# Kernel optimization log

Hardware: AMD Instinct MI355X
Metric: run time of the kernel (lower is better)

## Reference

```python
import jax, jax.numpy as jnp
import numpy as np

B, T, D_IN, H, C = 256, 2048, 64, 32, 16
RHO, SPARSITY = 0.9, 0.1


def _reservoir(rng, n):
    # uniform(-1,1), scale to spectral radius RHO, then sparsify (same order as torch code)
    W = rng.uniform(-1.0, 1.0, (n, n)).astype(np.float32)
    W *= RHO / np.max(np.abs(np.linalg.eigvals(W)))
    W *= (rng.random((n, n)) < SPARSITY).astype(np.float32)
    return jnp.asarray(W)


def _linear(rng, fan_in, fan_out):
    bound = 1.0 / np.sqrt(fan_in)
    W = rng.uniform(-bound, bound, (fan_out, fan_in)).astype(np.float32)
    b = rng.uniform(-bound, bound, (fan_out,)).astype(np.float32)
    return jnp.asarray(W), jnp.asarray(b)


def setup_inputs() -> dict:
    key = jax.random.key(0)
    rng = np.random.default_rng(0)
    x = jax.random.normal(key, (B, T, D_IN), dtype=jnp.float32)
    # frozen encoder input / reservoir weights (uniform(-1,1) weights, default-init biases)
    W_in = jnp.asarray(rng.uniform(-1.0, 1.0, (H, D_IN)).astype(np.float32))
    b_in = jnp.asarray(rng.uniform(-1 / np.sqrt(D_IN), 1 / np.sqrt(D_IN), (H,)).astype(np.float32))
    W_res_enc = _reservoir(rng, H)
    b_res_enc = jnp.asarray(rng.uniform(-1 / np.sqrt(H), 1 / np.sqrt(H), (H,)).astype(np.float32))
    W_code, b_code = _linear(rng, H, C)
    W_co, b_co = _linear(rng, C, H)
    W_res_dec = _reservoir(rng, H)
    b_res_dec = jnp.asarray(rng.uniform(-1 / np.sqrt(H), 1 / np.sqrt(H), (H,)).astype(np.float32))
    W_ro, b_ro = _linear(rng, H, D_IN)
    return dict(x=x, W_in=W_in, b_in=b_in, W_res_enc=W_res_enc, b_res_enc=b_res_enc,
                W_code=W_code, b_code=b_code, W_co=W_co, b_co=b_co,
                W_res_dec=W_res_dec, b_res_dec=b_res_dec, W_ro=W_ro, b_ro=b_ro)


def reference(x, W_in, b_in, W_res_enc, b_res_enc, W_code, b_code, W_co, b_co,
              W_res_dec, b_res_dec, W_ro, b_ro):
    Bs = x.shape[0]
    h0 = jnp.zeros((Bs, W_res_enc.shape[0]), dtype=x.dtype)
    # precompute input projection for all timesteps: [T, B, H]
    u_enc = jnp.swapaxes(jnp.einsum('btd,hd->bth', x, W_in) + b_in, 0, 1)

    def enc_step(h, u):
        h = jnp.tanh(u + h @ W_res_enc.T + b_res_enc)
        return h, h

    _, enc = jax.lax.scan(enc_step, h0, u_enc)
    enc = jnp.swapaxes(enc, 0, 1)                      # [B, T, H]

    z = enc @ W_code.T + b_code                        # [B, T, C]
    h_dec_in = z @ W_co.T + b_co                       # [B, T, H]

    def dec_step(h, u):
        h = jnp.tanh(u + h @ W_res_dec.T + b_res_dec)
        return h, h

    _, dec = jax.lax.scan(dec_step, h0, jnp.swapaxes(h_dec_in, 0, 1))
    dec = jnp.swapaxes(dec, 0, 1)                      # [B, T, H]
    return dec @ W_ro.T + b_ro                         # [B, T, D_IN]
```

## Files before the change

### kernel.cpp

```cpp
#include <hip/hip_runtime.h>
#include <math.h>

#define B_    256
#define T_    2048
#define DIN   64
#define H_    32
#define C_    16

#define CHUNK 128
#define WARM  96
#define NCHUNK (T_ / CHUNK)

#define OFF_WCOMB 0u
#define OFF_BCOMB 4096u
#define OFF_U     (1u << 20)

__device__ __forceinline__ float fast_tanh(float x) {
    float e2 = __expf(x + x);
    return 1.0f - 2.0f * __builtin_amdgcn_rcpf(e2 + 1.0f);
}

__global__ __launch_bounds__(1024) void prep_kernel(
        const float* __restrict__ W_code, const float* __restrict__ b_code,
        const float* __restrict__ W_co,   const float* __restrict__ b_co,
        float* __restrict__ W_comb, float* __restrict__ b_comb) {
    int t = threadIdx.x;
    int i = t >> 5, j = t & 31;
    float s = 0.0f;
#pragma unroll
    for (int c = 0; c < C_; ++c)
        s += W_co[i * C_ + c] * W_code[c * H_ + j];
    W_comb[i * H_ + j] = s;
    if (t < H_) {
        float sb = b_co[t];
#pragma unroll
        for (int c = 0; c < C_; ++c)
            sb += W_co[t * C_ + c] * b_code[c];
        b_comb[t] = sb;
    }
}

__global__ __launch_bounds__(256) void inproj_kernel(
        const float* __restrict__ x, const float* __restrict__ W_in,
        const float* __restrict__ b_in, const float* __restrict__ b_res_enc,
        float* __restrict__ u) {
    __shared__ __align__(16) float4 lx[128 * 16];

    int tid  = threadIdx.x;
    int w    = tid >> 6;
    int lane = tid & 63;
    int i    = lane & 31;
    int par  = lane >> 5;

    float Wr[DIN];
    {
        const float4* wi4 = reinterpret_cast<const float4*>(W_in + i * DIN);
#pragma unroll
        for (int q = 0; q < DIN / 4; ++q) {
            float4 v = wi4[q];
            Wr[4*q+0] = v.x; Wr[4*q+1] = v.y; Wr[4*q+2] = v.z; Wr[4*q+3] = v.w;
        }
    }
    float bi = b_in[i] + b_res_enc[i];

    long row_base = (long)blockIdx.x * 128;
    const float4* xg = reinterpret_cast<const float4*>(x) + row_base * 16;

#pragma unroll
    for (int k = 0; k < 8; ++k)
        lx[tid + 256 * k] = xg[tid + 256 * k];
    __syncthreads();

#pragma unroll
    for (int g = 0; g < 4; ++g) {
        int r0 = w * 32 + g * 8 + par;
        float acc0 = 0.f, acc1 = 0.f, acc2 = 0.f, acc3 = 0.f;
#pragma unroll
        for (int k4 = 0; k4 < 16; ++k4) {
            float4 wv = { Wr[4*k4+0], Wr[4*k4+1], Wr[4*k4+2], Wr[4*k4+3] };
            float4 x0 = lx[(r0 + 0) * 16 + k4];
            float4 x1 = lx[(r0 + 2) * 16 + k4];
            float4 x2 = lx[(r0 + 4) * 16 + k4];
            float4 x3 = lx[(r0 + 6) * 16 + k4];
            acc0 += x0.x * wv.x + x0.y * wv.y + x0.z * wv.z + x0.w * wv.w;
            acc1 += x1.x * wv.x + x1.y * wv.y + x1.z * wv.z + x1.w * wv.w;
            acc2 += x2.x * wv.x + x2.y * wv.y + x2.z * wv.z + x2.w * wv.w;
            acc3 += x3.x * wv.x + x3.y * wv.y + x3.z * wv.z + x3.w * wv.w;
        }
        long rg = row_base + r0;
        u[(rg + 0) * H_ + i] = acc0 + bi;
        u[(rg + 2) * H_ + i] = acc1 + bi;
        u[(rg + 4) * H_ + i] = acc2 + bi;
        u[(rg + 6) * H_ + i] = acc3 + bi;
    }
}

__device__ __forceinline__ float mv32(const float (&W)[H_], const float (&h)[H_],
                                      float init) {
    float a0 = init, a1 = 0.f, a2 = 0.f, a3 = 0.f;
#pragma unroll
    for (int j = 0; j < H_; j += 4) {
        a0 += W[j+0] * h[j+0];
        a1 += W[j+1] * h[j+1];
        a2 += W[j+2] * h[j+2];
        a3 += W[j+3] * h[j+3];
    }
    return (a0 + a1) + (a2 + a3);
}

__device__ __forceinline__ void gather32(const float (&src)[H_], float (&h)[H_]) {
#pragma unroll
    for (int q = 0; q < H_ / 4; ++q) {
        float4 v = *reinterpret_cast<const float4*>(&src[4 * q]);
        h[4*q+0] = v.x; h[4*q+1] = v.y; h[4*q+2] = v.z; h[4*q+3] = v.w;
    }
}

__device__ __forceinline__ void readout2(const float (&Wo0)[H_], const float (&Wo1)[H_],
                                         float bo0, float bo1, const float (&hd)[H_],
                                         float* dst) {
    float s00 = bo0, s01 = 0.f, s10 = bo1, s11 = 0.f;
#pragma unroll
    for (int j = 0; j < H_; j += 2) {
        s00 += Wo0[j]     * hd[j];
        s01 += Wo0[j + 1] * hd[j + 1];
        s10 += Wo1[j]     * hd[j];
        s11 += Wo1[j + 1] * hd[j + 1];
    }
    *reinterpret_cast<float2*>(dst) = make_float2(s00 + s01, s10 + s11);
}

__global__ __launch_bounds__(64, 2) void scan_kernel(
        const float* __restrict__ u,
        const float* __restrict__ W_res_enc,
        const float* __restrict__ W_res_dec, const float* __restrict__ b_res_dec,
        const float* __restrict__ W_comb,    const float* __restrict__ b_comb,
        const float* __restrict__ W_ro,      const float* __restrict__ b_ro,
        float* __restrict__ out) {
    int lane = threadIdx.x;
    int i = lane & 31;
    int half = lane >> 5;
    int b  = ((blockIdx.x & 127) << 1) | half;
    int c  = blockIdx.x >> 7;
    int t0 = c * CHUNK;
    int tstart = (c == 0) ? 0 : (t0 - WARM);
    int tend = t0 + CHUNK;

    float We[H_], Wc[H_], Wd[H_], Wo0[H_], Wo1[H_];
    {
        const float4* we4 = reinterpret_cast<const float4*>(W_res_enc + i * H_);
        const float4* wc4 = reinterpret_cast<const float4*>(W_comb + i * H_);
        const float4* wd4 = reinterpret_cast<const float4*>(W_res_dec + i * H_);
        const float4* wo0 = reinterpret_cast<const float4*>(W_ro + (2 * i) * H_);
        const float4* wo1 = reinterpret_cast<const float4*>(W_ro + (2 * i + 1) * H_);
#pragma unroll
        for (int q = 0; q < H_ / 4; ++q) {
            float4 a = we4[q], bq = wc4[q], d = wd4[q], o0 = wo0[q], o1 = wo1[q];
            We[4*q+0]=a.x;  We[4*q+1]=a.y;  We[4*q+2]=a.z;  We[4*q+3]=a.w;
            Wc[4*q+0]=bq.x; Wc[4*q+1]=bq.y; Wc[4*q+2]=bq.z; Wc[4*q+3]=bq.w;
            Wd[4*q+0]=d.x;  Wd[4*q+1]=d.y;  Wd[4*q+2]=d.z;  Wd[4*q+3]=d.w;
            Wo0[4*q+0]=o0.x;Wo0[4*q+1]=o0.y;Wo0[4*q+2]=o0.z;Wo0[4*q+3]=o0.w;
            Wo1[4*q+0]=o1.x;Wo1[4*q+1]=o1.y;Wo1[4*q+2]=o1.z;Wo1[4*q+3]=o1.w;
        }
    }
    float bcd = b_comb[i] + b_res_dec[i];
    float bo0 = b_ro[2 * i], bo1 = b_ro[2 * i + 1];

    float henc[H_], hdec[H_];
#pragma unroll
    for (int j = 0; j < H_; ++j) { henc[j] = 0.0f; hdec[j] = 0.0f; }

    __shared__ __align__(16) float lhe[2][H_];
    __shared__ __align__(16) float lhd[2][H_];

    const float* ub = u + ((long)b * T_) * H_ + i;
    float*       ob = out + ((long)b * T_) * DIN + 2 * i;

    float ucur = ub[(long)tstart * H_];
    float un1  = ub[(long)(tstart + 1) * H_];

    for (int t = tstart; t < t0; ++t) {
        float a = fast_tanh(mv32(We, henc, ucur));
        lhe[half][i] = a;
        gather32(lhe[half], henc);
        float dacc = mv32(Wd, hdec, 0.f);
        ucur = un1;
        un1 = ub[(t + 2) * H_];
        float d = fast_tanh(mv32(Wc, henc, bcd) + dacc);
        lhd[half][i] = d;
        gather32(lhd[half], hdec);
    }

    {
        float a = fast_tanh(mv32(We, henc, ucur));
        lhe[half][i] = a;
        gather32(lhe[half], henc);
        float dacc = mv32(Wd, hdec, 0.f);
        ucur = un1;
        un1 = ub[(t0 + 2) * H_];
        float d = fast_tanh(mv32(Wc, henc, bcd) + dacc);
        lhd[half][i] = d;
        gather32(lhd[half], hdec);
    }

    for (int t = t0 + 1; t < tend; ++t) {
        float a = fast_tanh(mv32(We, henc, ucur));
        lhe[half][i] = a;
        gather32(lhe[half], henc);
        float dacc = mv32(Wd, hdec, 0.f);
        readout2(Wo0, Wo1, bo0, bo1, hdec, ob + (long)(t - 1) * DIN);
        int tn = (t + 2 < tend) ? (t + 2) : (tend - 1);
        ucur = un1;
        un1 = ub[tn * H_];
        float d = fast_tanh(mv32(Wc, henc, bcd) + dacc);
        lhd[half][i] = d;
        gather32(lhd[half], hdec);
    }
    readout2(Wo0, Wo1, bo0, bo1, hdec, ob + (long)(tend - 1) * DIN);
}

extern "C" void kernel_launch(void* const* d_in, const int* in_sizes, int n_in,
                              void* d_out, int out_size, void* d_ws, size_t ws_size,
                              hipStream_t stream) {
    const float* x         = (const float*)d_in[0];
    const float* W_in      = (const float*)d_in[1];
    const float* b_in      = (const float*)d_in[2];
    const float* W_res_enc = (const float*)d_in[3];
    const float* b_res_enc = (const float*)d_in[4];
    const float* W_code    = (const float*)d_in[5];
    const float* b_code    = (const float*)d_in[6];
    const float* W_co      = (const float*)d_in[7];
    const float* b_co      = (const float*)d_in[8];
    const float* W_res_dec = (const float*)d_in[9];
    const float* b_res_dec = (const float*)d_in[10];
    const float* W_ro      = (const float*)d_in[11];
    const float* b_ro      = (const float*)d_in[12];
    float* out = (float*)d_out;

    char* ws = (char*)d_ws;
    float* W_comb = (float*)(ws + OFF_WCOMB);
    float* b_comb = (float*)(ws + OFF_BCOMB);
    float* u      = (float*)(ws + OFF_U);

    prep_kernel<<<1, 1024, 0, stream>>>(W_code, b_code, W_co, b_co, W_comb, b_comb);
    inproj_kernel<<<(B_ * T_) / 128, 256, 0, stream>>>(x, W_in, b_in, b_res_enc, u);
    scan_kernel<<<(B_ / 2) * NCHUNK, 64, 0, stream>>>(u, W_res_enc,
                                                      W_res_dec, b_res_dec,
                                                      W_comb, b_comb, W_ro, b_ro, out);
}
```

Baseline: 541.7 us.

## Split readout projection out of the scan into a separate output-projection kernel

Removes the per-step 64-wide readout from the latency-bound recurrent scan. The scan now writes the decoder hidden state into the first 32 floats of each output row, and a new kernel reads those back, applies W_ro and overwrites the row in place. This shortens the serial critical path and frees registers (launch bounds relaxed to 1 block per SIMD hint), and the input prefetch is deepened to three steps. The cost is an extra kernel launch plus a write and re-read of the hidden states through global memory. The in-place reuse of the output buffer relies on each block reading its rows into shared memory before any of them are overwritten.

Measured after the change: 533.9 us. Within noise of the previous version (-1.4%).

```diff
diff --git a/kernel.cpp b/kernel.cpp
--- a/kernel.cpp
+++ b/kernel.cpp
@@ -116,27 +116,12 @@
     }
 }
 
-__device__ __forceinline__ void readout2(const float (&Wo0)[H_], const float (&Wo1)[H_],
-                                         float bo0, float bo1, const float (&hd)[H_],
-                                         float* dst) {
-    float s00 = bo0, s01 = 0.f, s10 = bo1, s11 = 0.f;
-#pragma unroll
-    for (int j = 0; j < H_; j += 2) {
-        s00 += Wo0[j]     * hd[j];
-        s01 += Wo0[j + 1] * hd[j + 1];
-        s10 += Wo1[j]     * hd[j];
-        s11 += Wo1[j + 1] * hd[j + 1];
-    }
-    *reinterpret_cast<float2*>(dst) = make_float2(s00 + s01, s10 + s11);
-}
-
-__global__ __launch_bounds__(64, 2) void scan_kernel(
+__global__ __launch_bounds__(64, 1) void scan_kernel(
         const float* __restrict__ u,
         const float* __restrict__ W_res_enc,
         const float* __restrict__ W_res_dec, const float* __restrict__ b_res_dec,
         const float* __restrict__ W_comb,    const float* __restrict__ b_comb,
-        const float* __restrict__ W_ro,      const float* __restrict__ b_ro,
-        float* __restrict__ out) {
+        float* __restrict__ hd ) {
     int lane = threadIdx.x;
     int i = lane & 31;
     int half = lane >> 5;
@@ -146,25 +131,20 @@
     int tstart = (c == 0) ? 0 : (t0 - WARM);
     int tend = t0 + CHUNK;
 
-    float We[H_], Wc[H_], Wd[H_], Wo0[H_], Wo1[H_];
+    float We[H_], Wc[H_], Wd[H_];
     {
         const float4* we4 = reinterpret_cast<const float4*>(W_res_enc + i * H_);
         const float4* wc4 = reinterpret_cast<const float4*>(W_comb + i * H_);
         const float4* wd4 = reinterpret_cast<const float4*>(W_res_dec + i * H_);
-        const float4* wo0 = reinterpret_cast<const float4*>(W_ro + (2 * i) * H_);
-        const float4* wo1 = reinterpret_cast<const float4*>(W_ro + (2 * i + 1) * H_);
 #pragma unroll
         for (int q = 0; q < H_ / 4; ++q) {
-            float4 a = we4[q], bq = wc4[q], d = wd4[q], o0 = wo0[q], o1 = wo1[q];
+            float4 a = we4[q], bq = wc4[q], d = wd4[q];
             We[4*q+0]=a.x;  We[4*q+1]=a.y;  We[4*q+2]=a.z;  We[4*q+3]=a.w;
             Wc[4*q+0]=bq.x; Wc[4*q+1]=bq.y; Wc[4*q+2]=bq.z; Wc[4*q+3]=bq.w;
             Wd[4*q+0]=d.x;  Wd[4*q+1]=d.y;  Wd[4*q+2]=d.z;  Wd[4*q+3]=d.w;
-            Wo0[4*q+0]=o0.x;Wo0[4*q+1]=o0.y;Wo0[4*q+2]=o0.z;Wo0[4*q+3]=o0.w;
-            Wo1[4*q+0]=o1.x;Wo1[4*q+1]=o1.y;Wo1[4*q+2]=o1.z;Wo1[4*q+3]=o1.w;
         }
     }
     float bcd = b_comb[i] + b_res_dec[i];
-    float bo0 = b_ro[2 * i], bo1 = b_ro[2 * i + 1];
 
     float henc[H_], hdec[H_];
 #pragma unroll
@@ -174,49 +154,85 @@
     __shared__ __align__(16) float lhd[2][H_];
 
     const float* ub = u + ((long)b * T_) * H_ + i;
-    float*       ob = out + ((long)b * T_) * DIN + 2 * i;
+    float*       hb = hd + ((long)b * T_) * DIN + i;
 
     float ucur = ub[(long)tstart * H_];
     float un1  = ub[(long)(tstart + 1) * H_];
+    float un2  = ub[(long)(tstart + 2) * H_];
 
     for (int t = tstart; t < t0; ++t) {
         float a = fast_tanh(mv32(We, henc, ucur));
         lhe[half][i] = a;
         gather32(lhe[half], henc);
         float dacc = mv32(Wd, hdec, 0.f);
-        ucur = un1;
-        un1 = ub[(t + 2) * H_];
+        ucur = un1; un1 = un2;
+        un2 = ub[(t + 3) * H_];
         float d = fast_tanh(mv32(Wc, henc, bcd) + dacc);
         lhd[half][i] = d;
         gather32(lhd[half], hdec);
     }
 
-    {
+    for (int t = t0; t < tend; ++t) {
         float a = fast_tanh(mv32(We, henc, ucur));
         lhe[half][i] = a;
         gather32(lhe[half], henc);
         float dacc = mv32(Wd, hdec, 0.f);
-        ucur = un1;
-        un1 = ub[(t0 + 2) * H_];
+        int tn = t + 3; if (tn > tend - 1) tn = tend - 1;
+        ucur = un1; un1 = un2;
+        un2 = ub[(long)tn * H_];
         float d = fast_tanh(mv32(Wc, henc, bcd) + dacc);
+        hb[(long)t * DIN] = d;
         lhd[half][i] = d;
         gather32(lhd[half], hdec);
     }
-
-    for (int t = t0 + 1; t < tend; ++t) {
-        float a = fast_tanh(mv32(We, henc, ucur));
-        lhe[half][i] = a;
-        gather32(lhe[half], henc);
-        float dacc = mv32(Wd, hdec, 0.f);
-        readout2(Wo0, Wo1, bo0, bo1, hdec, ob + (long)(t - 1) * DIN);
-        int tn = (t + 2 < tend) ? (t + 2) : (tend - 1);
-        ucur = un1;
-        un1 = ub[tn * H_];
-        float d = fast_tanh(mv32(Wc, henc, bcd) + dacc);
-        lhd[half][i] = d;
-        gather32(lhd[half], hdec);
-    }
-    readout2(Wo0, Wo1, bo0, bo1, hdec, ob + (long)(tend - 1) * DIN);
+}
+
+__global__ __launch_bounds__(256) void outproj_kernel(
+        const float* __restrict__ W_ro, const float* __restrict__ b_ro,
+        float* __restrict__ out) {
+    __shared__ __align__(16) float4 lh[128 * 8];
+
+    int tid  = threadIdx.x;
+    int w    = tid >> 6;
+    int o    = tid & 63;
+
+    float Wo[H_];
+    {
+        const float4* wo4 = reinterpret_cast<const float4*>(W_ro + o * H_);
+#pragma unroll
+        for (int q = 0; q < H_ / 4; ++q) {
+            float4 v = wo4[q];
+            Wo[4*q+0] = v.x; Wo[4*q+1] = v.y; Wo[4*q+2] = v.z; Wo[4*q+3] = v.w;
+        }
+    }
+    float bo = b_ro[o];
+
+    long row_base = (long)blockIdx.x * 128;
+    const float4* hg = reinterpret_cast<const float4*>(out);
+
+#pragma unroll
+    for (int k = 0; k < 4; ++k) {
+        int idx = tid + 256 * k;
+        int r = idx >> 3, q = idx & 7;
+        lh[idx] = hg[(row_base + r) * 16 + q];
+    }
+    __syncthreads();
+
+    float* ob = out + (row_base + (long)w * 32) * DIN + o;
+#pragma unroll 4
+    for (int r = 0; r < 32; ++r) {
+        int rr = w * 32 + r;
+        float s0 = bo, s1 = 0.f, s2 = 0.f, s3 = 0.f;
+#pragma unroll
+        for (int q = 0; q < 8; ++q) {
+            float4 h4 = lh[rr * 8 + q];
+            s0 += Wo[4*q+0] * h4.x;
+            s1 += Wo[4*q+1] * h4.y;
+            s2 += Wo[4*q+2] * h4.z;
+            s3 += Wo[4*q+3] * h4.w;
+        }
+        __builtin_nontemporal_store((s0 + s1) + (s2 + s3), ob + (long)r * DIN);
+    }
 }
 
 extern "C" void kernel_launch(void* const* d_in, const int* in_sizes, int n_in,
@@ -246,5 +262,6 @@
     inproj_kernel<<<(B_ * T_) / 128, 256, 0, stream>>>(x, W_in, b_in, b_res_enc, u);
     scan_kernel<<<(B_ / 2) * NCHUNK, 64, 0, stream>>>(u, W_res_enc,
                                                       W_res_dec, b_res_dec,
-                                                      W_comb, b_comb, W_ro, b_ro, out);
-}
+                                                      W_comb, b_comb, out);
+    outproj_kernel<<<(B_ * T_) / 128, 256, 0, stream>>>(W_ro, b_ro, out);
+}
```
